# Optimization experiments

Measured on AMD Instinct MI355X. Metric: run time of the kernel, lower is better.

Reference implementation:

```python
import jax, jax.numpy as jnp
import numpy as np

B, T, N = 2048, 48, 32
DYN, STAT, H = 6, 5, 64
IN = DYN + STAT


def setup_inputs() -> dict:
    key = jax.random.key(0)
    ks = jax.random.split(key, 18)
    rn = lambda k, s: jax.random.normal(k, s, jnp.float32) * 0.05
    return {
        "x_history": jax.random.normal(ks[0], (B, T, N, IN), jnp.float32),
        "adj": jax.random.uniform(ks[1], (N, N), dtype=jnp.float32),
        "W_enc": rn(ks[2], (IN, H)), "b_enc": jnp.zeros((H,), jnp.float32),
        "W_g1": rn(ks[3], (H, H)), "b_g1": jnp.zeros((H,), jnp.float32),
        "W_g2": rn(ks[4], (H, H)), "b_g2": jnp.zeros((H,), jnp.float32),
        "W_ih": rn(ks[5], (4 * H, H)), "W_hh": rn(ks[6], (4 * H, H)),
        "b_ih": jnp.zeros((4 * H,), jnp.float32), "b_hh": jnp.zeros((4 * H,), jnp.float32),
        "W_d1": rn(ks[7], (H, H // 2)), "b_d1": jnp.zeros((H // 2,), jnp.float32),
        "W_d2": rn(ks[8], (H // 2, DYN)), "b_d2": jnp.zeros((DYN,), jnp.float32),
        "future_steps": 48,
    }


def _norm_adj(adj):
    # PyG DenseGCNConv: set self-loops to 1, symmetric D^-1/2 (A) D^-1/2
    n = adj.shape[0]
    a = adj.at[jnp.diag_indices(n)].set(1.0)
    d = jnp.clip(a.sum(-1), 1.0) ** -0.5
    return d[:, None] * a * d[None, :]


def reference(x_history, adj, W_enc, b_enc, W_g1, b_g1, W_g2, b_g2,
              W_ih, W_hh, b_ih, b_hh, W_d1, b_d1, W_d2, b_d2, future_steps):
    b, t, n, _ = x_history.shape
    h = W_enc.shape[1]
    dyn = W_d2.shape[1]
    Ahat = _norm_adj(adj)

    def spatial(x):  # x: [b, n, in] -> [b*n, h]
        enc = jax.nn.relu(x @ W_enc + b_enc)
        s = jax.nn.relu(jnp.einsum('ij,bjh->bih', Ahat, enc @ W_g1) + b_g1)
        s = jax.nn.relu(jnp.einsum('ij,bjh->bih', Ahat, s @ W_g2) + b_g2)
        return s.reshape(b * n, h)

    def lstm(xf, hx, cx):  # torch LSTMCell gate order: i, f, g, o
        g = xf @ W_ih.T + b_ih + hx @ W_hh.T + b_hh
        gi, gf, gg, go = jnp.split(g, 4, axis=-1)
        c = jax.nn.sigmoid(gf) * cx + jax.nn.sigmoid(gi) * jnp.tanh(gg)
        return jax.nn.sigmoid(go) * jnp.tanh(c), c

    hx = jnp.zeros((b * n, h), x_history.dtype)
    cx = jnp.zeros((b * n, h), x_history.dtype)

    def enc_step(carry, x_t):
        hx, cx = carry
        hx, cx = lstm(spatial(x_t), hx, cx)
        return (hx, cx), None

    (hx, cx), _ = jax.lax.scan(enc_step, (hx, cx), jnp.swapaxes(x_history, 0, 1))

    last = x_history[:, -1]  # [b, n, in]
    pred = last[..., :dyn]
    stat = last[..., dyn:]

    def dec_step(carry, _):
        pred, hx, cx = carry
        cur = jnp.concatenate([pred, stat], axis=-1)
        hx, cx = lstm(spatial(cur), hx, cx)
        hu = hx.reshape(b, n, h)
        res = jax.nn.relu(hu @ W_d1 + b_d1) @ W_d2 + b_d2
        pred = pred + res
        return (pred, hx, cx), pred

    _, outs = jax.lax.scan(dec_step, (pred, hx, cx), None, length=future_steps)
    return jnp.swapaxes(outs, 0, 1)  # [b, future_steps, n, dyn]
```

## Files before the change

kernel.cpp:

```cpp
#include <hip/hip_runtime.h>
#include <cstdint>


#define NT 512
#define TSTEPS 48
#define FUT 48

typedef __bf16 bf16;
typedef __attribute__((ext_vector_type(2))) __bf16 bf16x2;
typedef __attribute__((ext_vector_type(8))) __bf16 bf16x8;
typedef __attribute__((ext_vector_type(16))) float f32x16;
typedef unsigned int uint32x4v __attribute__((ext_vector_type(4)));

#define L2E  1.442695041f
#define L2E2 2.885390082f

__device__ __forceinline__ uint32_t pk2(float x, float y) {
  union { bf16x2 h; uint32_t u; } t;
  t.h[0] = (bf16)x; t.h[1] = (bf16)y;
  return t.u;
}

__device__ __forceinline__ bf16x8 cpack8(float v0, float v1, float v2, float v3,
                                         float v4, float v5, float v6, float v7) {
  uint32_t a0 = pk2(v0, v1), a1 = pk2(v2, v3);
  uint32_t b0 = pk2(v4, v5), b1 = pk2(v6, v7);
  auto r0 = __builtin_amdgcn_permlane32_swap(a0, b0, false, false);
  auto r1 = __builtin_amdgcn_permlane32_swap(a1, b1, false, false);
  union { uint32x4v u; bf16x8 h; } o;
  o.u = uint32x4v{(uint32_t)r0[0], (uint32_t)r1[0], (uint32_t)r0[1], (uint32_t)r1[1]};
  return o.h;
}

__global__ __launch_bounds__(NT, 2)
void stgnn_kernel(const float* __restrict__ xh, const float* __restrict__ adj,
                  const float* __restrict__ Wenc, const float* __restrict__ benc,
                  const float* __restrict__ Wg1, const float* __restrict__ bg1,
                  const float* __restrict__ Wg2, const float* __restrict__ bg2,
                  const float* __restrict__ Wih, const float* __restrict__ Whh,
                  const float* __restrict__ bih, const float* __restrict__ bhh,
                  const float* __restrict__ Wd1, const float* __restrict__ bd1,
                  const float* __restrict__ Wd2, const float* __restrict__ bd2,
                  float* __restrict__ out) {
  __shared__ __align__(16) bf16 wcatTA[32768];
  __shared__ __align__(16) bf16 wg1B[4096];
  __shared__ __align__(16) bf16 wg2B[4096];
  __shared__ __align__(16) bf16 wencTA[1024];
  __shared__ __align__(16) bf16 wd1TA[2048];
  __shared__ __align__(16) bf16 wd2TA[1024];
  __shared__ __align__(16) bf16 ahHiB[1024];
  __shared__ __align__(16) bf16 ahLoB[1024];
  __shared__ __align__(16) float sBg1[64];
  __shared__ __align__(16) float sBg2[64];
  __shared__ __align__(16) float sBih[256];
  __shared__ __align__(16) float sBd1[32];
  __shared__ __align__(16) float sBd2[8];
  __shared__ float sDeg[32];
  __shared__ __align__(16) float sAh[1024];

  const int tid = threadIdx.x;
  const int L   = tid & 63;
  const int w   = tid >> 6;
  const int n5  = L & 31;
  const int hf  = L >> 5;
  const long long b = (long long)blockIdx.x * 8 + w;

  for (int i = tid; i < 1024; i += NT) {
    int f = i >> 6, h = i & 63;
    float v = (f < 11) ? Wenc[f * 64 + h] : (f == 11 ? benc[h] : 0.0f);
    wencTA[(h >> 5) * 512 + ((h & 31) + 32 * ((f >> 3) & 1)) * 8 + (f & 7)] = (bf16)v;
  }
  for (int i = tid; i < 4096; i += NT) {
    int k = i >> 6, n = i & 63;
    int off = (((n >> 5) * 4 + (k >> 4)) * 64 + (n & 31) + 32 * ((k >> 3) & 1)) * 8 + (k & 7);
    wg1B[off] = (bf16)Wg1[i];
    wg2B[off] = (bf16)Wg2[i];
  }
  for (int i = tid; i < 32768; i += NT) {
    int gc = i >> 7, k = i & 127;
    float v = (k < 64) ? Wih[gc * 64 + k] : Whh[gc * 64 + (k - 64)];
    wcatTA[((gc >> 5) * 8 + (k >> 4)) * 512 + ((gc & 31) + 32 * ((k >> 3) & 1)) * 8 + (k & 7)] = (bf16)v;
  }
  for (int i = tid; i < 2048; i += NT) {
    int k = i >> 5, n = i & 31;
    wd1TA[(k >> 4) * 512 + (n + 32 * ((k >> 3) & 1)) * 8 + (k & 7)] = (bf16)Wd1[k * 32 + n];
  }
  for (int i = tid; i < 1024; i += NT) {
    int k = i >> 5, d = i & 31;
    float v = (d < 6) ? Wd2[k * 6 + d] : 0.0f;
    wd2TA[(k >> 4) * 512 + (d + 32 * ((k >> 3) & 1)) * 8 + (k & 7)] = (bf16)v;
  }
  for (int i = tid; i < 64; i += NT) { sBg1[i] = bg1[i]; sBg2[i] = bg2[i]; }
  for (int i = tid; i < 256; i += NT) sBih[i] = bih[i] + bhh[i];
  for (int i = tid; i < 32; i += NT) sBd1[i] = bd1[i];
  if (tid < 8) sBd2[tid] = (tid < 6) ? bd2[tid] : 0.0f;
  if (tid < 32) {
    float s = 0.0f;
    for (int j = 0; j < 32; ++j) s += (j == tid) ? 1.0f : adj[tid * 32 + j];
    sDeg[tid] = 1.0f / sqrtf(fmaxf(s, 1.0f));
  }
  __syncthreads();
  for (int i = tid; i < 1024; i += NT) {
    int ii = i >> 5, jj = i & 31;
    float v = (ii == jj) ? 1.0f : adj[i];
    sAh[i] = sDeg[ii] * v * sDeg[jj];
  }
  __syncthreads();
  if (w == 0) {
    #pragma unroll
    for (int c = 0; c < 2; ++c)
      #pragma unroll
      for (int j = 0; j < 8; ++j) {
        int k = 16 * c + 8 * hf + j;
        float v = sAh[n5 * 32 + k];
        bf16 hi = (bf16)v;
        ahHiB[c * 512 + L * 8 + j] = hi;
        ahLoB[c * 512 + L * 8 + j] = (bf16)(v - (float)hi);
      }
  }
  __syncthreads();

  const bf16x8 aH0 = *reinterpret_cast<const bf16x8*>(&ahHiB[L * 8]);
  const bf16x8 aL0 = *reinterpret_cast<const bf16x8*>(&ahLoB[L * 8]);
  const bf16x8 aH1 = *reinterpret_cast<const bf16x8*>(&ahHiB[512 + L * 8]);
  const bf16x8 aL1 = *reinterpret_cast<const bf16x8*>(&ahLoB[512 + L * 8]);
  const bf16x8 wencR0 = *reinterpret_cast<const bf16x8*>(&wencTA[L * 8]);
  const bf16x8 wencR1 = *reinterpret_cast<const bf16x8*>(&wencTA[512 + L * 8]);
  bf16x8 wg1R[8], wg2R[8];
  #pragma unroll
  for (int c = 0; c < 8; ++c) {
    wg1R[c] = *reinterpret_cast<const bf16x8*>(&wg1B[c * 512 + L * 8]);
    wg2R[c] = *reinterpret_cast<const bf16x8*>(&wg2B[c * 512 + L * 8]);
  }

  float cx[32];
  #pragma unroll
  for (int i = 0; i < 32; ++i) cx[i] = 0.0f;
  bf16x8 xfhB[8];
  #pragma unroll
  for (int t = 0; t < 8; ++t)
    #pragma unroll
    for (int j = 0; j < 8; ++j) xfhB[t][j] = (bf16)0.0f;
  float predr[4] = {0.f, 0.f, 0.f, 0.f};
  float st0 = 0.f, st1 = 0.f, st2 = 0.f;

  float fx0, fx1, fx2, fx3, fx4, fx5, fx6, fx7;
  auto LOADX = [&](int s) {
    const float* px = xh + b * (TSTEPS * 352LL) + (long long)s * 352 + n5 * 11 + (hf << 3);
    fx0 = px[0]; fx1 = px[1]; fx2 = px[2];
    fx3 = fx4 = fx5 = fx6 = fx7 = 0.0f;
    if (!hf) { fx3 = px[3]; fx4 = px[4]; fx5 = px[5]; fx6 = px[6]; fx7 = px[7]; }
  };
  auto PACKX = [&]() -> bf16x8 {
    uint32_t d0 = pk2(fx0, fx1);
    uint32_t d1 = hf ? pk2(fx2, 1.0f) : pk2(fx2, fx3);
    uint32_t d2 = hf ? 0u : pk2(fx4, fx5);
    uint32_t d3 = hf ? 0u : pk2(fx6, fx7);
    union { uint32x4v u; bf16x8 h; } xo;
    xo.u = uint32x4v{d0, d1, d2, d3};
    return xo.h;
  };
  LOADX(0);
  bf16x8 xBcur = PACKX();
  LOADX(1);

  #pragma unroll 1
  for (int step = 0; step < TSTEPS + FUT; ++step) {
    asm volatile("" ::: "memory");
    const bool de = (step >= TSTEPS);
    const bf16x8 xB = xBcur;
    if (!de) {
      if (step + 1 < TSTEPS) xBcur = PACKX();
      if (step + 2 < TSTEPS) LOADX(step + 2);
    }
    bf16x8 rA[4];
    #pragma unroll
    for (int mt = 0; mt < 2; ++mt) {
      f32x16 c;
      #pragma unroll
      for (int i = 0; i < 16; ++i) c[i] = 0.0f;
      c = __builtin_amdgcn_mfma_f32_32x32x16_bf16(mt ? wencR1 : wencR0, xB, c, 0, 0, 0);
      rA[2*mt]   = cpack8(fmaxf(c[0], 0.f), fmaxf(c[1], 0.f), fmaxf(c[2], 0.f), fmaxf(c[3], 0.f),
                          fmaxf(c[4], 0.f), fmaxf(c[5], 0.f), fmaxf(c[6], 0.f), fmaxf(c[7], 0.f));
      rA[2*mt+1] = cpack8(fmaxf(c[8], 0.f), fmaxf(c[9], 0.f), fmaxf(c[10], 0.f), fmaxf(c[11], 0.f),
                          fmaxf(c[12], 0.f), fmaxf(c[13], 0.f), fmaxf(c[14], 0.f), fmaxf(c[15], 0.f));
    }
    bf16x8 nA[4];
    #pragma unroll
    for (int nt = 0; nt < 2; ++nt) {
      f32x16 c;
      #pragma unroll
      for (int i = 0; i < 16; ++i) c[i] = 0.0f;
      #pragma unroll
      for (int cc = 0; cc < 4; ++cc)
        c = __builtin_amdgcn_mfma_f32_32x32x16_bf16(rA[cc], wg1R[nt * 4 + cc], c, 0, 0, 0);
      nA[2*nt]   = cpack8(c[0], c[1], c[2], c[3], c[4], c[5], c[6], c[7]);
      nA[2*nt+1] = cpack8(c[8], c[9], c[10], c[11], c[12], c[13], c[14], c[15]);
    }
    #pragma unroll
    for (int mt = 0; mt < 2; ++mt) {
      f32x16 c;
      #pragma unroll
      for (int g = 0; g < 4; ++g) {
        float4 bb = *reinterpret_cast<const float4*>(&sBg1[32 * mt + 8 * g + 4 * hf]);
        c[4*g+0] = bb.x; c[4*g+1] = bb.y; c[4*g+2] = bb.z; c[4*g+3] = bb.w;
      }
      c = __builtin_amdgcn_mfma_f32_32x32x16_bf16(nA[mt * 2 + 0], aH0, c, 0, 0, 0);
      c = __builtin_amdgcn_mfma_f32_32x32x16_bf16(nA[mt * 2 + 0], aL0, c, 0, 0, 0);
      c = __builtin_amdgcn_mfma_f32_32x32x16_bf16(nA[mt * 2 + 1], aH1, c, 0, 0, 0);
      c = __builtin_amdgcn_mfma_f32_32x32x16_bf16(nA[mt * 2 + 1], aL1, c, 0, 0, 0);
      rA[2*mt]   = cpack8(fmaxf(c[0], 0.f), fmaxf(c[1], 0.f), fmaxf(c[2], 0.f), fmaxf(c[3], 0.f),
                          fmaxf(c[4], 0.f), fmaxf(c[5], 0.f), fmaxf(c[6], 0.f), fmaxf(c[7], 0.f));
      rA[2*mt+1] = cpack8(fmaxf(c[8], 0.f), fmaxf(c[9], 0.f), fmaxf(c[10], 0.f), fmaxf(c[11], 0.f),
                          fmaxf(c[12], 0.f), fmaxf(c[13], 0.f), fmaxf(c[14], 0.f), fmaxf(c[15], 0.f));
    }
    #pragma unroll
    for (int nt = 0; nt < 2; ++nt) {
      f32x16 c;
      #pragma unroll
      for (int i = 0; i < 16; ++i) c[i] = 0.0f;
      #pragma unroll
      for (int cc = 0; cc < 4; ++cc)
        c = __builtin_amdgcn_mfma_f32_32x32x16_bf16(rA[cc], wg2R[nt * 4 + cc], c, 0, 0, 0);
      nA[2*nt]   = cpack8(c[0], c[1], c[2], c[3], c[4], c[5], c[6], c[7]);
      nA[2*nt+1] = cpack8(c[8], c[9], c[10], c[11], c[12], c[13], c[14], c[15]);
    }
    #pragma unroll
    for (int mt = 0; mt < 2; ++mt) {
      f32x16 c;
      #pragma unroll
      for (int g = 0; g < 4; ++g) {
        float4 bb = *reinterpret_cast<const float4*>(&sBg2[32 * mt + 8 * g + 4 * hf]);
        c[4*g+0] = bb.x; c[4*g+1] = bb.y; c[4*g+2] = bb.z; c[4*g+3] = bb.w;
      }
      c = __builtin_amdgcn_mfma_f32_32x32x16_bf16(nA[mt * 2 + 0], aH0, c, 0, 0, 0);
      c = __builtin_amdgcn_mfma_f32_32x32x16_bf16(nA[mt * 2 + 0], aL0, c, 0, 0, 0);
      c = __builtin_amdgcn_mfma_f32_32x32x16_bf16(nA[mt * 2 + 1], aH1, c, 0, 0, 0);
      c = __builtin_amdgcn_mfma_f32_32x32x16_bf16(nA[mt * 2 + 1], aL1, c, 0, 0, 0);
      xfhB[2*mt]   = cpack8(fmaxf(c[0], 0.f), fmaxf(c[1], 0.f), fmaxf(c[2], 0.f), fmaxf(c[3], 0.f),
                            fmaxf(c[4], 0.f), fmaxf(c[5], 0.f), fmaxf(c[6], 0.f), fmaxf(c[7], 0.f));
      xfhB[2*mt+1] = cpack8(fmaxf(c[8], 0.f), fmaxf(c[9], 0.f), fmaxf(c[10], 0.f), fmaxf(c[11], 0.f),
                            fmaxf(c[12], 0.f), fmaxf(c[13], 0.f), fmaxf(c[14], 0.f), fmaxf(c[15], 0.f));
    }
    bf16x8 hN[4];
    #pragma unroll
    for (int p = 0; p < 2; ++p) {
      f32x16 gI, gG;
      #pragma unroll
      for (int g = 0; g < 4; ++g) {
        float4 bI = *reinterpret_cast<const float4*>(&sBih[      32 * p + 8 * g + 4 * hf]);
        float4 bG = *reinterpret_cast<const float4*>(&sBih[128 + 32 * p + 8 * g + 4 * hf]);
        gI[4*g+0]=bI.x; gI[4*g+1]=bI.y; gI[4*g+2]=bI.z; gI[4*g+3]=bI.w;
        gG[4*g+0]=bG.x; gG[4*g+1]=bG.y; gG[4*g+2]=bG.z; gG[4*g+3]=bG.w;
      }
      #pragma unroll
      for (int cc = 0; cc < 8; ++cc) {
        gI = __builtin_amdgcn_mfma_f32_32x32x16_bf16(
               *reinterpret_cast<const bf16x8*>(&wcatTA[((0 + p) * 8 + cc) * 512 + L * 8]),
               xfhB[cc], gI, 0, 0, 0);
        gG = __builtin_amdgcn_mfma_f32_32x32x16_bf16(
               *reinterpret_cast<const bf16x8*>(&wcatTA[((4 + p) * 8 + cc) * 512 + L * 8]),
               xfhB[cc], gG, 0, 0, 0);
      }
      float term[16];
      #pragma unroll
      for (int ri = 0; ri < 16; ++ri) {
        float ei = __builtin_amdgcn_exp2f(gI[ri] * -L2E);
        float eg = __builtin_amdgcn_exp2f(gG[ri] * L2E2);
        float A  = 1.0f + ei;
        float T  = __builtin_fmaf(A, eg, A);
        term[ri] = (eg - 1.0f) * __builtin_amdgcn_rcpf(T);
      }
      f32x16 gF;
      #pragma unroll
      for (int g = 0; g < 4; ++g) {
        float4 bF = *reinterpret_cast<const float4*>(&sBih[64 + 32 * p + 8 * g + 4 * hf]);
        gF[4*g+0]=bF.x; gF[4*g+1]=bF.y; gF[4*g+2]=bF.z; gF[4*g+3]=bF.w;
      }
      #pragma unroll
      for (int cc = 0; cc < 8; ++cc)
        gF = __builtin_amdgcn_mfma_f32_32x32x16_bf16(
               *reinterpret_cast<const bf16x8*>(&wcatTA[((2 + p) * 8 + cc) * 512 + L * 8]),
               xfhB[cc], gF, 0, 0, 0);
      #pragma unroll
      for (int ri = 0; ri < 16; ++ri) {
        float ef = __builtin_amdgcn_exp2f(gF[ri] * -L2E);
        cx[p * 16 + ri] = __builtin_fmaf(cx[p * 16 + ri],
                            __builtin_amdgcn_rcpf(1.0f + ef), term[ri]);
      }
      f32x16 gO;
      #pragma unroll
      for (int g = 0; g < 4; ++g) {
        float4 bO = *reinterpret_cast<const float4*>(&sBih[192 + 32 * p + 8 * g + 4 * hf]);
        gO[4*g+0]=bO.x; gO[4*g+1]=bO.y; gO[4*g+2]=bO.z; gO[4*g+3]=bO.w;
      }
      #pragma unroll
      for (int cc = 0; cc < 8; ++cc)
        gO = __builtin_amdgcn_mfma_f32_32x32x16_bf16(
               *reinterpret_cast<const bf16x8*>(&wcatTA[((6 + p) * 8 + cc) * 512 + L * 8]),
               xfhB[cc], gO, 0, 0, 0);
      float hq[16];
      #pragma unroll
      for (int ri = 0; ri < 16; ++ri) {
        float eo = __builtin_amdgcn_exp2f(gO[ri] * -L2E);
        float ec = __builtin_amdgcn_exp2f(cx[p * 16 + ri] * L2E2);
        float B1 = 1.0f + eo;
        float T2 = __builtin_fmaf(B1, ec, B1);
        hq[ri] = (ec - 1.0f) * __builtin_amdgcn_rcpf(T2);
      }
      hN[2*p]   = cpack8(hq[0], hq[1], hq[2], hq[3], hq[4], hq[5], hq[6], hq[7]);
      hN[2*p+1] = cpack8(hq[8], hq[9], hq[10], hq[11], hq[12], hq[13], hq[14], hq[15]);
    }
    #pragma unroll
    for (int t = 0; t < 4; ++t) xfhB[4 + t] = hN[t];
    if (de) {
      if (step == TSTEPS) {
        const float* px = xh + ((b * TSTEPS + (TSTEPS - 1)) * 32 + n5) * 11;
        if (hf == 0) { predr[0] = px[0]; predr[1] = px[1]; predr[2] = px[2]; predr[3] = px[3]; }
        else         { predr[0] = px[4]; predr[1] = px[5]; }
        st0 = px[6 + 2 * hf]; st1 = px[7 + 2 * hf]; st2 = px[10];
      }
      f32x16 cD;
      #pragma unroll
      for (int g = 0; g < 4; ++g) {
        float4 bb = *reinterpret_cast<const float4*>(&sBd1[8 * g + 4 * hf]);
        cD[4*g+0] = bb.x; cD[4*g+1] = bb.y; cD[4*g+2] = bb.z; cD[4*g+3] = bb.w;
      }
      #pragma unroll
      for (int cc = 0; cc < 4; ++cc)
        cD = __builtin_amdgcn_mfma_f32_32x32x16_bf16(
               *reinterpret_cast<const bf16x8*>(&wd1TA[cc * 512 + L * 8]), xfhB[4 + cc], cD, 0, 0, 0);
      bf16x8 rB0 = cpack8(fmaxf(cD[0], 0.f), fmaxf(cD[1], 0.f), fmaxf(cD[2], 0.f), fmaxf(cD[3], 0.f),
                          fmaxf(cD[4], 0.f), fmaxf(cD[5], 0.f), fmaxf(cD[6], 0.f), fmaxf(cD[7], 0.f));
      bf16x8 rB1 = cpack8(fmaxf(cD[8], 0.f), fmaxf(cD[9], 0.f), fmaxf(cD[10], 0.f), fmaxf(cD[11], 0.f),
                          fmaxf(cD[12], 0.f), fmaxf(cD[13], 0.f), fmaxf(cD[14], 0.f), fmaxf(cD[15], 0.f));
      f32x16 c2;
      #pragma unroll
      for (int i = 0; i < 4; ++i) c2[i] = sBd2[4 * hf + i];
      #pragma unroll
      for (int i = 4; i < 16; ++i) c2[i] = 0.0f;
      c2 = __builtin_amdgcn_mfma_f32_32x32x16_bf16(
             *reinterpret_cast<const bf16x8*>(&wd2TA[L * 8]), rB0, c2, 0, 0, 0);
      c2 = __builtin_amdgcn_mfma_f32_32x32x16_bf16(
             *reinterpret_cast<const bf16x8*>(&wd2TA[512 + L * 8]), rB1, c2, 0, 0, 0);
      float* op = out + ((b * FUT + (step - TSTEPS)) * 32 + n5) * 6;
      if (hf == 0) {
        float p0 = predr[0] + c2[0];
        float p1 = predr[1] + c2[1];
        float p2 = predr[2] + c2[2];
        float p3 = predr[3] + c2[3];
        predr[0] = p0; predr[1] = p1; predr[2] = p2; predr[3] = p3;
        *reinterpret_cast<float2*>(op + 0) = make_float2(p0, p1);
        *reinterpret_cast<float2*>(op + 2) = make_float2(p2, p3);
      } else {
        float p4 = predr[0] + c2[0];
        float p5 = predr[1] + c2[1];
        predr[0] = p4; predr[1] = p5;
        *reinterpret_cast<float2*>(op + 4) = make_float2(p4, p5);
      }
      uint32_t pa = pk2(predr[0], predr[1]);
      auto sw = __builtin_amdgcn_permlane32_swap(pa, pa, false, false);
      uint32_t d0 = hf ? pk2(st0, st1)  : pa;
      uint32_t d1 = hf ? pk2(st2, 1.0f) : pk2(predr[2], predr[3]);
      uint32_t d2 = hf ? 0u : (uint32_t)sw[1];
      uint32_t d3 = hf ? 0u : pk2(st0, st1);
      union { uint32x4v u; bf16x8 h; } xo;
      xo.u = uint32x4v{d0, d1, d2, d3};
      xBcur = xo.h;
    }
  }
}

extern "C" void kernel_launch(void* const* d_in, const int* in_sizes, int n_in,
                              void* d_out, int out_size, void* d_ws, size_t ws_size,
                              hipStream_t stream) {
  (void)in_sizes; (void)n_in; (void)d_ws; (void)ws_size; (void)out_size;
  const float* xh   = (const float*)d_in[0];
  const float* adj  = (const float*)d_in[1];
  const float* Wenc = (const float*)d_in[2];
  const float* benc = (const float*)d_in[3];
  const float* Wg1  = (const float*)d_in[4];
  const float* bg1  = (const float*)d_in[5];
  const float* Wg2  = (const float*)d_in[6];
  const float* bg2  = (const float*)d_in[7];
  const float* Wih  = (const float*)d_in[8];
  const float* Whh  = (const float*)d_in[9];
  const float* bih  = (const float*)d_in[10];
  const float* bhh  = (const float*)d_in[11];
  const float* Wd1  = (const float*)d_in[12];
  const float* bd1  = (const float*)d_in[13];
  const float* Wd2  = (const float*)d_in[14];
  const float* bd2  = (const float*)d_in[15];
  float* out = (float*)d_out;
  stgnn_kernel<<<dim3(256), dim3(NT), 0, stream>>>(
      xh, adj, Wenc, benc, Wg1, bg1, Wg2, bg2,
      Wih, Whh, bih, bhh, Wd1, bd1, Wd2, bd2, out);
}
```

Measured before the change: 966.2 us.

## Software-pipeline encoder: overlap next step's GCN chain with current LSTM gates

Splits the single fused loop into separate encoder and decoder loops. In the encoder, the spatial GCN chain for step s+1 is computed first (prologue) and then interleaved with the LSTM gate MFMAs and transcendental math of step s, so independent work can hide dependency latency. GCN weights wg1/wg2 are now read from LDS per use instead of being held in registers, which frees VGPRs but adds LDS traffic. The x load is also made branchless, and the decoder keeps the serial order.

```diff
diff --git a/kernel.cpp b/kernel.cpp
--- a/kernel.cpp
+++ b/kernel.cpp
@@ -126,12 +126,6 @@
   const bf16x8 aL1 = *reinterpret_cast<const bf16x8*>(&ahLoB[512 + L * 8]);
   const bf16x8 wencR0 = *reinterpret_cast<const bf16x8*>(&wencTA[L * 8]);
   const bf16x8 wencR1 = *reinterpret_cast<const bf16x8*>(&wencTA[512 + L * 8]);
-  bf16x8 wg1R[8], wg2R[8];
-  #pragma unroll
-  for (int c = 0; c < 8; ++c) {
-    wg1R[c] = *reinterpret_cast<const bf16x8*>(&wg1B[c * 512 + L * 8]);
-    wg2R[c] = *reinterpret_cast<const bf16x8*>(&wg2B[c * 512 + L * 8]);
-  }
 
   float cx[32];
   #pragma unroll
@@ -144,12 +138,131 @@
   float predr[4] = {0.f, 0.f, 0.f, 0.f};
   float st0 = 0.f, st1 = 0.f, st2 = 0.f;
 
+  auto RELUPK = [&](const f32x16& c, bf16x8& o0, bf16x8& o1) {
+    o0 = cpack8(fmaxf(c[0], 0.f), fmaxf(c[1], 0.f), fmaxf(c[2], 0.f), fmaxf(c[3], 0.f),
+                fmaxf(c[4], 0.f), fmaxf(c[5], 0.f), fmaxf(c[6], 0.f), fmaxf(c[7], 0.f));
+    o1 = cpack8(fmaxf(c[8], 0.f), fmaxf(c[9], 0.f), fmaxf(c[10], 0.f), fmaxf(c[11], 0.f),
+                fmaxf(c[12], 0.f), fmaxf(c[13], 0.f), fmaxf(c[14], 0.f), fmaxf(c[15], 0.f));
+  };
+  auto RAWPK = [&](const f32x16& c, bf16x8& o0, bf16x8& o1) {
+    o0 = cpack8(c[0], c[1], c[2], c[3], c[4], c[5], c[6], c[7]);
+    o1 = cpack8(c[8], c[9], c[10], c[11], c[12], c[13], c[14], c[15]);
+  };
+  auto ST_ENC = [&](const bf16x8& xB, bf16x8* rA) {
+    #pragma unroll
+    for (int mt = 0; mt < 2; ++mt) {
+      f32x16 c;
+      #pragma unroll
+      for (int i = 0; i < 16; ++i) c[i] = 0.0f;
+      c = __builtin_amdgcn_mfma_f32_32x32x16_bf16(mt ? wencR1 : wencR0, xB, c, 0, 0, 0);
+      RELUPK(c, rA[2*mt], rA[2*mt+1]);
+    }
+  };
+  auto ST_MUL = [&](const bf16* wB, const bf16x8* rA, bf16x8* nA) {
+    #pragma unroll
+    for (int nt = 0; nt < 2; ++nt) {
+      f32x16 c;
+      #pragma unroll
+      for (int i = 0; i < 16; ++i) c[i] = 0.0f;
+      #pragma unroll
+      for (int cc = 0; cc < 4; ++cc)
+        c = __builtin_amdgcn_mfma_f32_32x32x16_bf16(rA[cc],
+              *reinterpret_cast<const bf16x8*>(&wB[(nt * 4 + cc) * 512 + L * 8]), c, 0, 0, 0);
+      RAWPK(c, nA[2*nt], nA[2*nt+1]);
+    }
+  };
+  auto ST_AH = [&](const float* sBias, const bf16x8* nA, bf16x8* rA) {
+    #pragma unroll
+    for (int mt = 0; mt < 2; ++mt) {
+      f32x16 c;
+      #pragma unroll
+      for (int g = 0; g < 4; ++g) {
+        float4 bb = *reinterpret_cast<const float4*>(&sBias[32 * mt + 8 * g + 4 * hf]);
+        c[4*g+0] = bb.x; c[4*g+1] = bb.y; c[4*g+2] = bb.z; c[4*g+3] = bb.w;
+      }
+      c = __builtin_amdgcn_mfma_f32_32x32x16_bf16(nA[mt * 2 + 0], aH0, c, 0, 0, 0);
+      c = __builtin_amdgcn_mfma_f32_32x32x16_bf16(nA[mt * 2 + 0], aL0, c, 0, 0, 0);
+      c = __builtin_amdgcn_mfma_f32_32x32x16_bf16(nA[mt * 2 + 1], aH1, c, 0, 0, 0);
+      c = __builtin_amdgcn_mfma_f32_32x32x16_bf16(nA[mt * 2 + 1], aL1, c, 0, 0, 0);
+      RELUPK(c, rA[2*mt], rA[2*mt+1]);
+    }
+  };
+  auto CHAIN = [&](const bf16x8& xB, bf16x8* xfN) {
+    bf16x8 rA[4], nA[4];
+    ST_ENC(xB, rA);
+    ST_MUL(wg1B, rA, nA);
+    ST_AH(sBg1, nA, rA);
+    ST_MUL(wg2B, rA, nA);
+    ST_AH(sBg2, nA, xfN);
+  };
+  auto GATE2 = [&](int p, int gidx0, int gidx1, f32x16& gA, f32x16& gB) {
+    #pragma unroll
+    for (int g = 0; g < 4; ++g) {
+      float4 bA = *reinterpret_cast<const float4*>(&sBih[gidx0 * 64 + 32 * p + 8 * g + 4 * hf]);
+      float4 bBv = *reinterpret_cast<const float4*>(&sBih[gidx1 * 64 + 32 * p + 8 * g + 4 * hf]);
+      gA[4*g+0]=bA.x; gA[4*g+1]=bA.y; gA[4*g+2]=bA.z; gA[4*g+3]=bA.w;
+      gB[4*g+0]=bBv.x; gB[4*g+1]=bBv.y; gB[4*g+2]=bBv.z; gB[4*g+3]=bBv.w;
+    }
+    #pragma unroll
+    for (int cc = 0; cc < 8; ++cc) {
+      gA = __builtin_amdgcn_mfma_f32_32x32x16_bf16(
+             *reinterpret_cast<const bf16x8*>(&wcatTA[((gidx0 * 2 + p) * 8 + cc) * 512 + L * 8]),
+             xfhB[cc], gA, 0, 0, 0);
+      gB = __builtin_amdgcn_mfma_f32_32x32x16_bf16(
+             *reinterpret_cast<const bf16x8*>(&wcatTA[((gidx1 * 2 + p) * 8 + cc) * 512 + L * 8]),
+             xfhB[cc], gB, 0, 0, 0);
+    }
+  };
+  auto GATE1 = [&](int p, int gidx, f32x16& gX) {
+    #pragma unroll
+    for (int g = 0; g < 4; ++g) {
+      float4 bb = *reinterpret_cast<const float4*>(&sBih[gidx * 64 + 32 * p + 8 * g + 4 * hf]);
+      gX[4*g+0]=bb.x; gX[4*g+1]=bb.y; gX[4*g+2]=bb.z; gX[4*g+3]=bb.w;
+    }
+    #pragma unroll
+    for (int cc = 0; cc < 8; ++cc)
+      gX = __builtin_amdgcn_mfma_f32_32x32x16_bf16(
+             *reinterpret_cast<const bf16x8*>(&wcatTA[((gidx * 2 + p) * 8 + cc) * 512 + L * 8]),
+             xfhB[cc], gX, 0, 0, 0);
+  };
+  auto TERM = [&](const f32x16& gI, const f32x16& gG, float* term) {
+    #pragma unroll
+    for (int ri = 0; ri < 16; ++ri) {
+      float ei = __builtin_amdgcn_exp2f(gI[ri] * -L2E);
+      float eg = __builtin_amdgcn_exp2f(gG[ri] * L2E2);
+      float A  = 1.0f + ei;
+      float T  = __builtin_fmaf(A, eg, A);
+      term[ri] = (eg - 1.0f) * __builtin_amdgcn_rcpf(T);
+    }
+  };
+  auto CUPD = [&](int p, const f32x16& gF, const float* term) {
+    #pragma unroll
+    for (int ri = 0; ri < 16; ++ri) {
+      float ef = __builtin_amdgcn_exp2f(gF[ri] * -L2E);
+      cx[p * 16 + ri] = __builtin_fmaf(cx[p * 16 + ri],
+                          __builtin_amdgcn_rcpf(1.0f + ef), term[ri]);
+    }
+  };
+  auto HOUT = [&](int p, const f32x16& gO, bf16x8& h0, bf16x8& h1) {
+    float hq[16];
+    #pragma unroll
+    for (int ri = 0; ri < 16; ++ri) {
+      float eo = __builtin_amdgcn_exp2f(gO[ri] * -L2E);
+      float ec = __builtin_amdgcn_exp2f(cx[p * 16 + ri] * L2E2);
+      float B1 = 1.0f + eo;
+      float T2 = __builtin_fmaf(B1, ec, B1);
+      hq[ri] = (ec - 1.0f) * __builtin_amdgcn_rcpf(T2);
+    }
+    h0 = cpack8(hq[0], hq[1], hq[2], hq[3], hq[4], hq[5], hq[6], hq[7]);
+    h1 = cpack8(hq[8], hq[9], hq[10], hq[11], hq[12], hq[13], hq[14], hq[15]);
+  };
+
   float fx0, fx1, fx2, fx3, fx4, fx5, fx6, fx7;
   auto LOADX = [&](int s) {
     const float* px = xh + b * (TSTEPS * 352LL) + (long long)s * 352 + n5 * 11 + (hf << 3);
+    const float* q  = hf ? px - 8 : px;
     fx0 = px[0]; fx1 = px[1]; fx2 = px[2];
-    fx3 = fx4 = fx5 = fx6 = fx7 = 0.0f;
-    if (!hf) { fx3 = px[3]; fx4 = px[4]; fx5 = px[5]; fx6 = px[6]; fx7 = px[7]; }
+    fx3 = q[3]; fx4 = q[4]; fx5 = q[5]; fx6 = q[6]; fx7 = q[7];
   };
   auto PACKX = [&]() -> bf16x8 {
     uint32_t d0 = pk2(fx0, fx1);
@@ -160,214 +273,135 @@
     xo.u = uint32x4v{d0, d1, d2, d3};
     return xo.h;
   };
+  auto BUILD_DECX = [&]() -> bf16x8 {
+    uint32_t pa = pk2(predr[0], predr[1]);
+    auto sw = __builtin_amdgcn_permlane32_swap(pa, pa, false, false);
+    uint32_t d0 = hf ? pk2(st0, st1)  : pa;
+    uint32_t d1 = hf ? pk2(st2, 1.0f) : pk2(predr[2], predr[3]);
+    uint32_t d2 = hf ? 0u : (uint32_t)sw[1];
+    uint32_t d3 = hf ? 0u : pk2(st0, st1);
+    union { uint32x4v u; bf16x8 h; } xo;
+    xo.u = uint32x4v{d0, d1, d2, d3};
+    return xo.h;
+  };
+
   LOADX(0);
+  {
+    bf16x8 xB0 = PACKX();
+    bf16x8 xfN[4];
+    CHAIN(xB0, xfN);
+    #pragma unroll
+    for (int t = 0; t < 4; ++t) xfhB[t] = xfN[t];
+  }
+  LOADX(1);
   bf16x8 xBcur = PACKX();
-  LOADX(1);
+  LOADX(2);
 
   #pragma unroll 1
-  for (int step = 0; step < TSTEPS + FUT; ++step) {
+  for (int s = 0; s < TSTEPS; ++s) {
     asm volatile("" ::: "memory");
-    const bool de = (step >= TSTEPS);
-    const bf16x8 xB = xBcur;
-    if (!de) {
-      if (step + 1 < TSTEPS) xBcur = PACKX();
-      if (step + 2 < TSTEPS) LOADX(step + 2);
-    }
-    bf16x8 rA[4];
-    #pragma unroll
-    for (int mt = 0; mt < 2; ++mt) {
-      f32x16 c;
-      #pragma unroll
-      for (int i = 0; i < 16; ++i) c[i] = 0.0f;
-      c = __builtin_amdgcn_mfma_f32_32x32x16_bf16(mt ? wencR1 : wencR0, xB, c, 0, 0, 0);
-      rA[2*mt]   = cpack8(fmaxf(c[0], 0.f), fmaxf(c[1], 0.f), fmaxf(c[2], 0.f), fmaxf(c[3], 0.f),
-                          fmaxf(c[4], 0.f), fmaxf(c[5], 0.f), fmaxf(c[6], 0.f), fmaxf(c[7], 0.f));
-      rA[2*mt+1] = cpack8(fmaxf(c[8], 0.f), fmaxf(c[9], 0.f), fmaxf(c[10], 0.f), fmaxf(c[11], 0.f),
-                          fmaxf(c[12], 0.f), fmaxf(c[13], 0.f), fmaxf(c[14], 0.f), fmaxf(c[15], 0.f));
-    }
-    bf16x8 nA[4];
-    #pragma unroll
-    for (int nt = 0; nt < 2; ++nt) {
-      f32x16 c;
-      #pragma unroll
-      for (int i = 0; i < 16; ++i) c[i] = 0.0f;
-      #pragma unroll
-      for (int cc = 0; cc < 4; ++cc)
-        c = __builtin_amdgcn_mfma_f32_32x32x16_bf16(rA[cc], wg1R[nt * 4 + cc], c, 0, 0, 0);
-      nA[2*nt]   = cpack8(c[0], c[1], c[2], c[3], c[4], c[5], c[6], c[7]);
-      nA[2*nt+1] = cpack8(c[8], c[9], c[10], c[11], c[12], c[13], c[14], c[15]);
-    }
-    #pragma unroll
-    for (int mt = 0; mt < 2; ++mt) {
-      f32x16 c;
-      #pragma unroll
-      for (int g = 0; g < 4; ++g) {
-        float4 bb = *reinterpret_cast<const float4*>(&sBg1[32 * mt + 8 * g + 4 * hf]);
-        c[4*g+0] = bb.x; c[4*g+1] = bb.y; c[4*g+2] = bb.z; c[4*g+3] = bb.w;
-      }
-      c = __builtin_amdgcn_mfma_f32_32x32x16_bf16(nA[mt * 2 + 0], aH0, c, 0, 0, 0);
-      c = __builtin_amdgcn_mfma_f32_32x32x16_bf16(nA[mt * 2 + 0], aL0, c, 0, 0, 0);
-      c = __builtin_amdgcn_mfma_f32_32x32x16_bf16(nA[mt * 2 + 1], aH1, c, 0, 0, 0);
-      c = __builtin_amdgcn_mfma_f32_32x32x16_bf16(nA[mt * 2 + 1], aL1, c, 0, 0, 0);
-      rA[2*mt]   = cpack8(fmaxf(c[0], 0.f), fmaxf(c[1], 0.f), fmaxf(c[2], 0.f), fmaxf(c[3], 0.f),
-                          fmaxf(c[4], 0.f), fmaxf(c[5], 0.f), fmaxf(c[6], 0.f), fmaxf(c[7], 0.f));
-      rA[2*mt+1] = cpack8(fmaxf(c[8], 0.f), fmaxf(c[9], 0.f), fmaxf(c[10], 0.f), fmaxf(c[11], 0.f),
-                          fmaxf(c[12], 0.f), fmaxf(c[13], 0.f), fmaxf(c[14], 0.f), fmaxf(c[15], 0.f));
-    }
-    #pragma unroll
-    for (int nt = 0; nt < 2; ++nt) {
-      f32x16 c;
-      #pragma unroll
-      for (int i = 0; i < 16; ++i) c[i] = 0.0f;
-      #pragma unroll
-      for (int cc = 0; cc < 4; ++cc)
-        c = __builtin_amdgcn_mfma_f32_32x32x16_bf16(rA[cc], wg2R[nt * 4 + cc], c, 0, 0, 0);
-      nA[2*nt]   = cpack8(c[0], c[1], c[2], c[3], c[4], c[5], c[6], c[7]);
-      nA[2*nt+1] = cpack8(c[8], c[9], c[10], c[11], c[12], c[13], c[14], c[15]);
-    }
-    #pragma unroll
-    for (int mt = 0; mt < 2; ++mt) {
-      f32x16 c;
-      #pragma unroll
-      for (int g = 0; g < 4; ++g) {
-        float4 bb = *reinterpret_cast<const float4*>(&sBg2[32 * mt + 8 * g + 4 * hf]);
-        c[4*g+0] = bb.x; c[4*g+1] = bb.y; c[4*g+2] = bb.z; c[4*g+3] = bb.w;
-      }
-      c = __builtin_amdgcn_mfma_f32_32x32x16_bf16(nA[mt * 2 + 0], aH0, c, 0, 0, 0);
-      c = __builtin_amdgcn_mfma_f32_32x32x16_bf16(nA[mt * 2 + 0], aL0, c, 0, 0, 0);
-      c = __builtin_amdgcn_mfma_f32_32x32x16_bf16(nA[mt * 2 + 1], aH1, c, 0, 0, 0);
-      c = __builtin_amdgcn_mfma_f32_32x32x16_bf16(nA[mt * 2 + 1], aL1, c, 0, 0, 0);
-      xfhB[2*mt]   = cpack8(fmaxf(c[0], 0.f), fmaxf(c[1], 0.f), fmaxf(c[2], 0.f), fmaxf(c[3], 0.f),
-                            fmaxf(c[4], 0.f), fmaxf(c[5], 0.f), fmaxf(c[6], 0.f), fmaxf(c[7], 0.f));
-      xfhB[2*mt+1] = cpack8(fmaxf(c[8], 0.f), fmaxf(c[9], 0.f), fmaxf(c[10], 0.f), fmaxf(c[11], 0.f),
-                            fmaxf(c[12], 0.f), fmaxf(c[13], 0.f), fmaxf(c[14], 0.f), fmaxf(c[15], 0.f));
-    }
+    f32x16 gI0, gG0;
+    GATE2(0, 0, 2, gI0, gG0);
+    bf16x8 rA[4], nA[4], xfN[4];
+    ST_ENC(xBcur, rA);
+    ST_MUL(wg1B, rA, nA);
+    f32x16 gF0;
+    GATE1(0, 1, gF0);
+    float term0[16];
+    TERM(gI0, gG0, term0);
+    ST_AH(sBg1, nA, rA);
+    ST_MUL(wg2B, rA, nA);
+    f32x16 gO0;
+    GATE1(0, 3, gO0);
+    CUPD(0, gF0, term0);
+    bf16x8 hN[4];
+    HOUT(0, gO0, hN[0], hN[1]);
+    ST_AH(sBg2, nA, xfN);
+    f32x16 gI1, gG1;
+    GATE2(1, 0, 2, gI1, gG1);
+    f32x16 gF1;
+    GATE1(1, 1, gF1);
+    float term1[16];
+    TERM(gI1, gG1, term1);
+    f32x16 gO1;
+    GATE1(1, 3, gO1);
+    CUPD(1, gF1, term1);
+    HOUT(1, gO1, hN[2], hN[3]);
+    #pragma unroll
+    for (int t = 0; t < 4; ++t) { xfhB[t] = xfN[t]; xfhB[4 + t] = hN[t]; }
+    xBcur = PACKX();
+    int nsl = (s + 3 < TSTEPS) ? s + 3 : TSTEPS - 1;
+    LOADX(nsl);
+  }
+
+  {
+    const float* px = xh + ((b * TSTEPS + (TSTEPS - 1)) * 32 + n5) * 11;
+    if (hf == 0) { predr[0] = px[0]; predr[1] = px[1]; predr[2] = px[2]; predr[3] = px[3]; }
+    else         { predr[0] = px[4]; predr[1] = px[5]; }
+    st0 = px[6 + 2 * hf]; st1 = px[7 + 2 * hf]; st2 = px[10];
+    xBcur = BUILD_DECX();
+  }
+
+  #pragma unroll 1
+  for (int s = 0; s < FUT; ++s) {
+    asm volatile("" ::: "memory");
+    bf16x8 xfN[4];
+    CHAIN(xBcur, xfN);
+    #pragma unroll
+    for (int t = 0; t < 4; ++t) xfhB[t] = xfN[t];
     bf16x8 hN[4];
     #pragma unroll
     for (int p = 0; p < 2; ++p) {
       f32x16 gI, gG;
-      #pragma unroll
-      for (int g = 0; g < 4; ++g) {
-        float4 bI = *reinterpret_cast<const float4*>(&sBih[      32 * p + 8 * g + 4 * hf]);
-        float4 bG = *reinterpret_cast<const float4*>(&sBih[128 + 32 * p + 8 * g + 4 * hf]);
-        gI[4*g+0]=bI.x; gI[4*g+1]=bI.y; gI[4*g+2]=bI.z; gI[4*g+3]=bI.w;
-        gG[4*g+0]=bG.x; gG[4*g+1]=bG.y; gG[4*g+2]=bG.z; gG[4*g+3]=bG.w;
-      }
-      #pragma unroll
-      for (int cc = 0; cc < 8; ++cc) {
-        gI = __builtin_amdgcn_mfma_f32_32x32x16_bf16(
-               *reinterpret_cast<const bf16x8*>(&wcatTA[((0 + p) * 8 + cc) * 512 + L * 8]),
-               xfhB[cc], gI, 0, 0, 0);
-        gG = __builtin_amdgcn_mfma_f32_32x32x16_bf16(
-               *reinterpret_cast<const bf16x8*>(&wcatTA[((4 + p) * 8 + cc) * 512 + L * 8]),
-               xfhB[cc], gG, 0, 0, 0);
-      }
+      GATE2(p, 0, 2, gI, gG);
       float term[16];
-      #pragma unroll
-      for (int ri = 0; ri < 16; ++ri) {
-        float ei = __builtin_amdgcn_exp2f(gI[ri] * -L2E);
-        float eg = __builtin_amdgcn_exp2f(gG[ri] * L2E2);
-        float A  = 1.0f + ei;
-        float T  = __builtin_fmaf(A, eg, A);
-        term[ri] = (eg - 1.0f) * __builtin_amdgcn_rcpf(T);
-      }
+      TERM(gI, gG, term);
       f32x16 gF;
-      #pragma unroll
-      for (int g = 0; g < 4; ++g) {
-        float4 bF = *reinterpret_cast<const float4*>(&sBih[64 + 32 * p + 8 * g + 4 * hf]);
-        gF[4*g+0]=bF.x; gF[4*g+1]=bF.y; gF[4*g+2]=bF.z; gF[4*g+3]=bF.w;
-      }
-      #pragma unroll
-      for (int cc = 0; cc < 8; ++cc)
-        gF = __builtin_amdgcn_mfma_f32_32x32x16_bf16(
-               *reinterpret_cast<const bf16x8*>(&wcatTA[((2 + p) * 8 + cc) * 512 + L * 8]),
-               xfhB[cc], gF, 0, 0, 0);
-      #pragma unroll
-      for (int ri = 0; ri < 16; ++ri) {
-        float ef = __builtin_amdgcn_exp2f(gF[ri] * -L2E);
-        cx[p * 16 + ri] = __builtin_fmaf(cx[p * 16 + ri],
-                            __builtin_amdgcn_rcpf(1.0f + ef), term[ri]);
-      }
+      GATE1(p, 1, gF);
+      CUPD(p, gF, term);
       f32x16 gO;
-      #pragma unroll
-      for (int g = 0; g < 4; ++g) {
-        float4 bO = *reinterpret_cast<const float4*>(&sBih[192 + 32 * p + 8 * g + 4 * hf]);
-        gO[4*g+0]=bO.x; gO[4*g+1]=bO.y; gO[4*g+2]=bO.z; gO[4*g+3]=bO.w;
-      }
-      #pragma unroll
-      for (int cc = 0; cc < 8; ++cc)
-        gO = __builtin_amdgcn_mfma_f32_32x32x16_bf16(
-               *reinterpret_cast<const bf16x8*>(&wcatTA[((6 + p) * 8 + cc) * 512 + L * 8]),
-               xfhB[cc], gO, 0, 0, 0);
-      float hq[16];
-      #pragma unroll
-      for (int ri = 0; ri < 16; ++ri) {
-        float eo = __builtin_amdgcn_exp2f(gO[ri] * -L2E);
-        float ec = __builtin_amdgcn_exp2f(cx[p * 16 + ri] * L2E2);
-        float B1 = 1.0f + eo;
-        float T2 = __builtin_fmaf(B1, ec, B1);
-        hq[ri] = (ec - 1.0f) * __builtin_amdgcn_rcpf(T2);
-      }
-      hN[2*p]   = cpack8(hq[0], hq[1], hq[2], hq[3], hq[4], hq[5], hq[6], hq[7]);
-      hN[2*p+1] = cpack8(hq[8], hq[9], hq[10], hq[11], hq[12], hq[13], hq[14], hq[15]);
+      GATE1(p, 3, gO);
+      HOUT(p, gO, hN[2*p], hN[2*p+1]);
     }
     #pragma unroll
     for (int t = 0; t < 4; ++t) xfhB[4 + t] = hN[t];
-    if (de) {
-      if (step == TSTEPS) {
-        const float* px = xh + ((b * TSTEPS + (TSTEPS - 1)) * 32 + n5) * 11;
-        if (hf == 0) { predr[0] = px[0]; predr[1] = px[1]; predr[2] = px[2]; predr[3] = px[3]; }
-        else         { predr[0] = px[4]; predr[1] = px[5]; }
-        st0 = px[6 + 2 * hf]; st1 = px[7 + 2 * hf]; st2 = px[10];
-      }
-      f32x16 cD;
-      #pragma unroll
-      for (int g = 0; g < 4; ++g) {
-        float4 bb = *reinterpret_cast<const float4*>(&sBd1[8 * g + 4 * hf]);
-        cD[4*g+0] = bb.x; cD[4*g+1] = bb.y; cD[4*g+2] = bb.z; cD[4*g+3] = bb.w;
-      }
-      #pragma unroll
-      for (int cc = 0; cc < 4; ++cc)
-        cD = __builtin_amdgcn_mfma_f32_32x32x16_bf16(
-               *reinterpret_cast<const bf16x8*>(&wd1TA[cc * 512 + L * 8]), xfhB[4 + cc], cD, 0, 0, 0);
-      bf16x8 rB0 = cpack8(fmaxf(cD[0], 0.f), fmaxf(cD[1], 0.f), fmaxf(cD[2], 0.f), fmaxf(cD[3], 0.f),
-                          fmaxf(cD[4], 0.f), fmaxf(cD[5], 0.f), fmaxf(cD[6], 0.f), fmaxf(cD[7], 0.f));
-      bf16x8 rB1 = cpack8(fmaxf(cD[8], 0.f), fmaxf(cD[9], 0.f), fmaxf(cD[10], 0.f), fmaxf(cD[11], 0.f),
-                          fmaxf(cD[12], 0.f), fmaxf(cD[13], 0.f), fmaxf(cD[14], 0.f), fmaxf(cD[15], 0.f));
-      f32x16 c2;
-      #pragma unroll
-      for (int i = 0; i < 4; ++i) c2[i] = sBd2[4 * hf + i];
-      #pragma unroll
-      for (int i = 4; i < 16; ++i) c2[i] = 0.0f;
-      c2 = __builtin_amdgcn_mfma_f32_32x32x16_bf16(
-             *reinterpret_cast<const bf16x8*>(&wd2TA[L * 8]), rB0, c2, 0, 0, 0);
-      c2 = __builtin_amdgcn_mfma_f32_32x32x16_bf16(
-             *reinterpret_cast<const bf16x8*>(&wd2TA[512 + L * 8]), rB1, c2, 0, 0, 0);
-      float* op = out + ((b * FUT + (step - TSTEPS)) * 32 + n5) * 6;
-      if (hf == 0) {
-        float p0 = predr[0] + c2[0];
-        float p1 = predr[1] + c2[1];
-        float p2 = predr[2] + c2[2];
-        float p3 = predr[3] + c2[3];
-        predr[0] = p0; predr[1] = p1; predr[2] = p2; predr[3] = p3;
-        *reinterpret_cast<float2*>(op + 0) = make_float2(p0, p1);
-        *reinterpret_cast<float2*>(op + 2) = make_float2(p2, p3);
-      } else {
-        float p4 = predr[0] + c2[0];
-        float p5 = predr[1] + c2[1];
-        predr[0] = p4; predr[1] = p5;
-        *reinterpret_cast<float2*>(op + 4) = make_float2(p4, p5);
-      }
-      uint32_t pa = pk2(predr[0], predr[1]);
-      auto sw = __builtin_amdgcn_permlane32_swap(pa, pa, false, false);
-      uint32_t d0 = hf ? pk2(st0, st1)  : pa;
-      uint32_t d1 = hf ? pk2(st2, 1.0f) : pk2(predr[2], predr[3]);
-      uint32_t d2 = hf ? 0u : (uint32_t)sw[1];
-      uint32_t d3 = hf ? 0u : pk2(st0, st1);
-      union { uint32x4v u; bf16x8 h; } xo;
-      xo.u = uint32x4v{d0, d1, d2, d3};
-      xBcur = xo.h;
-    }
+    f32x16 cD;
+    #pragma unroll
+    for (int g = 0; g < 4; ++g) {
+      float4 bb = *reinterpret_cast<const float4*>(&sBd1[8 * g + 4 * hf]);
+      cD[4*g+0] = bb.x; cD[4*g+1] = bb.y; cD[4*g+2] = bb.z; cD[4*g+3] = bb.w;
+    }
+    #pragma unroll
+    for (int cc = 0; cc < 4; ++cc)
+      cD = __builtin_amdgcn_mfma_f32_32x32x16_bf16(
+             *reinterpret_cast<const bf16x8*>(&wd1TA[cc * 512 + L * 8]), xfhB[4 + cc], cD, 0, 0, 0);
+    bf16x8 rB0, rB1;
+    RELUPK(cD, rB0, rB1);
+    f32x16 c2;
+    #pragma unroll
+    for (int i = 0; i < 4; ++i) c2[i] = sBd2[4 * hf + i];
+    #pragma unroll
+    for (int i = 4; i < 16; ++i) c2[i] = 0.0f;
+    c2 = __builtin_amdgcn_mfma_f32_32x32x16_bf16(
+           *reinterpret_cast<const bf16x8*>(&wd2TA[L * 8]), rB0, c2, 0, 0, 0);
+    c2 = __builtin_amdgcn_mfma_f32_32x32x16_bf16(
+           *reinterpret_cast<const bf16x8*>(&wd2TA[512 + L * 8]), rB1, c2, 0, 0, 0);
+    float* op = out + ((b * FUT + s) * 32 + n5) * 6;
+    if (hf == 0) {
+      float p0 = predr[0] + c2[0];
+      float p1 = predr[1] + c2[1];
+      float p2 = predr[2] + c2[2];
+      float p3 = predr[3] + c2[3];
+      predr[0] = p0; predr[1] = p1; predr[2] = p2; predr[3] = p3;
+      *reinterpret_cast<float2*>(op + 0) = make_float2(p0, p1);
+      *reinterpret_cast<float2*>(op + 2) = make_float2(p2, p3);
+    } else {
+      float p4 = predr[0] + c2[0];
+      float p5 = predr[1] + c2[1];
+      predr[0] = p4; predr[1] = p5;
+      *reinterpret_cast<float2*>(op + 4) = make_float2(p4, p5);
+    }
+    xBcur = BUILD_DECX();
   }
 }
 
```

After: 924.1 us. -4.4%, faster.
